# Kernel tuning notes

Hardware: AMD Instinct MI355X
Metric: run time of the kernel (lower is better)

Reference implementation:

```python
import jax, jax.numpy as jnp
import numpy as np

N = 50000
E = 800000
IN_DIM = 128
HID = 128
HEADS = 8
OUT_DIM = 64
NEG_SLOPE = 0.2


def setup_inputs() -> dict:
    key = jax.random.key(0)
    ks = jax.random.split(key, 12)
    x = jax.random.normal(ks[0], (N, IN_DIM), dtype=jnp.float32)
    edge_index = jax.random.randint(ks[1], (2, E), 0, N, dtype=jnp.int64)
    C1 = HID // HEADS  # per-head out dim of layer 1
    s1 = 1.0 / np.sqrt(IN_DIM)
    s2 = 1.0 / np.sqrt(HID)
    W1 = jax.random.uniform(ks[2], (IN_DIM, HEADS * C1), jnp.float32, -s1, s1)
    a_src1 = jax.random.uniform(ks[3], (HEADS, C1), jnp.float32, -1.0, 1.0)
    a_dst1 = jax.random.uniform(ks[4], (HEADS, C1), jnp.float32, -1.0, 1.0)
    b1 = jnp.zeros((HEADS * C1,), jnp.float32)
    W2 = jax.random.uniform(ks[5], (HID, OUT_DIM), jnp.float32, -s2, s2)
    a_src2 = jax.random.uniform(ks[6], (1, OUT_DIM), jnp.float32, -1.0, 1.0)
    a_dst2 = jax.random.uniform(ks[7], (1, OUT_DIM), jnp.float32, -1.0, 1.0)
    b2 = jnp.zeros((OUT_DIM,), jnp.float32)
    return {"x": x, "edge_index": edge_index, "W1": W1, "a_src1": a_src1,
            "a_dst1": a_dst1, "b1": b1, "W2": W2, "a_src2": a_src2,
            "a_dst2": a_dst2, "b2": b2}


def gat_conv(x, src, dst, W, a_s, a_d, b, n_heads, c_head):
    # Linear projection per head: [N, H, C]
    h = (x @ W).reshape(N, n_heads, c_head)
    # Per-node attention terms: [N, H]
    alpha_s = jnp.einsum('nhc,hc->nh', h, a_s)
    alpha_d = jnp.einsum('nhc,hc->nh', h, a_d)
    # Per-edge raw scores: [Etot, H]
    score = jax.nn.leaky_relu(alpha_s[src] + alpha_d[dst], negative_slope=NEG_SLOPE)
    # Segment softmax over edges sharing the same destination
    m = jax.ops.segment_max(score, dst, num_segments=N)
    e = jnp.exp(score - m[dst])
    denom = jax.ops.segment_sum(e, dst, num_segments=N)
    alpha = e / denom[dst]  # every node has a self-loop -> denom > 0
    # Weighted aggregation: scatter-add alpha * h_src into destinations
    out = jax.ops.segment_sum(alpha[:, :, None] * h[src], dst, num_segments=N)
    return out.reshape(N, n_heads * c_head) + b


def reference(x, edge_index, W1, a_src1, a_dst1, b1, W2, a_src2, a_dst2, b2):
    # add self loops (GATConv add_self_loops=True)
    loops = jnp.arange(N, dtype=edge_index.dtype)
    src = jnp.concatenate([edge_index[0], loops])
    dst = jnp.concatenate([edge_index[1], loops])
    C1 = HID // HEADS
    h = gat_conv(x, src, dst, W1, a_src1, a_dst1, b1, HEADS, C1)
    h = jax.nn.elu(h)  # dropout = 0 (eval)
    out = gat_conv(h, src, dst, W2, a_src2, a_dst2, b2, 1, OUT_DIM)
    return jax.nn.log_softmax(out, axis=-1)
```

## Files before the change

kernel.cpp:

```cpp
#include <hip/hip_runtime.h>
#include <math.h>

typedef unsigned int  u32;
typedef unsigned short u16;
typedef unsigned char u8;
typedef short bf16x8 __attribute__((ext_vector_type(8)));
typedef float f32x4  __attribute__((ext_vector_type(4)));
typedef float f32x2  __attribute__((ext_vector_type(2)));

#define NN    50000
#define NE    800000
#define ET    (NE + NN)
#define IND   128
#define HIDD  128
#define NH    8
#define OD    64
#define SLOPE 0.2f

#define NB    196
#define EPB   4096
#define NBB   ((NE + EPB - 1) / EPB)
#define LCAP  64
#define CAPB  5120
#define CPAD  16
#define BSTRIDE 7168

#define W1EXT 144
#define W2EXT 80
#define WPB   112
#define G1B   391

__device__ __forceinline__ u32 bf16rne(float f) {
    u32 u = __float_as_uint(f);
    return (u + 0x7fffu + ((u >> 16) & 1u)) >> 16;
}

#define LR(s) fmaxf((s), SLOPE * (s))

__global__ __launch_bounds__(256) void k_prep_bin(
    const int* __restrict__ ei, int* __restrict__ cnt, u32* __restrict__ staging,
    const float* __restrict__ W1, const float* __restrict__ W2,
    const float* __restrict__ as1w, const float* __restrict__ ad1w,
    const float* __restrict__ as2w, const float* __restrict__ ad2w,
    u16* __restrict__ Wt1, u16* __restrict__ Wt2,
    u32* __restrict__ h1f8, float* __restrict__ as1, float* __restrict__ as2)
{
    __shared__ u32 lbuf[NB * LCAP];
    __shared__ int lcnt[NB];
    __shared__ int gbase[NB];
    const int t = threadIdx.x;

    if (blockIdx.x >= NBB) {
        const int i = (blockIdx.x - NBB) * 256 + t;
        if (i < 32) h1f8[(size_t)NN * 32 + i] = 0;
        if (i < 8)  as1[(size_t)NH * NN + i] = -1e30f;
        if (i == 8) as2[NN] = -1e30f;

        if (i < W1EXT * 128) {
            const int j = i >> 7, k = i & 127;
            float v;
            if (j < 128) {
                v = W1[k * 128 + j];
            } else if (j < 136) {
                const int h = j - 128;
                v = 0.f;
                for (int c = 0; c < 16; ++c)
                    v += W1[k * 128 + h * 16 + c] * as1w[h * 16 + c];
            } else {
                const int h = j - 136;
                v = 0.f;
                for (int c = 0; c < 16; ++c)
                    v += W1[k * 128 + h * 16 + c] * ad1w[h * 16 + c];
            }
            Wt1[j * 128 + k] = (u16)bf16rne(v);
        } else if (i < W1EXT * 128 + W2EXT * 128) {
            const int i2 = i - W1EXT * 128;
            const int j = i2 >> 7, k = i2 & 127;
            float v = 0.f;
            if (j < 64) {
                v = W2[k * 64 + j];
            } else if (j == 64) {
                for (int c = 0; c < 64; ++c) v += W2[k * 64 + c] * as2w[c];
            } else if (j == 65) {
                for (int c = 0; c < 64; ++c) v += W2[k * 64 + c] * ad2w[c];
            }
            Wt2[j * 128 + k] = (u16)bf16rne(v);
        }
        return;
    }

    const int e0 = blockIdx.x * EPB;
    for (int i = t; i < NB; i += 256) lcnt[i] = 0;
    __syncthreads();

    for (int i = t; i < EPB; i += 256) {
        const int e = e0 + i;
        if (e >= NE) break;
        const int src = ei[e];
        const int dst = ei[NE + e];
        const int b = dst >> 8;
        const int p = atomicAdd(&lcnt[b], 1);
        lbuf[b * LCAP + p] = ((u32)(dst & 255) << 16) | (u32)src;
    }
    __syncthreads();

    for (int i = t; i < NB; i += 256)
        gbase[i] = atomicAdd(&cnt[i * CPAD], lcnt[i]);
    __syncthreads();

    for (int b = t; b < NB; b += 256) {
        const int n = lcnt[b];
        const int gb = gbase[b];
        u32* dstp = staging + (size_t)b * CAPB + gb;
        const u32* srcp = lbuf + b * LCAP;
        for (int j = 0; j < n; ++j) dstp[j] = srcp[j];
    }
}

__global__ __launch_bounds__(512) void k_place_gemm1(
    const int* __restrict__ cnt, const u32* __restrict__ staging,
    int* __restrict__ rowptr, int* __restrict__ rowend,
    u16* __restrict__ sorted16,
    const float* __restrict__ x, const u16* __restrict__ Wt1,
    u32* __restrict__ h1f8, float* __restrict__ as1, float* __restrict__ ad1)
{
    __shared__ u32 xb[128 * 64];
    __shared__ u32 Wb[W1EXT * 64];
    const int tid = threadIdx.x;

    if (blockIdx.x < NB) {
        int* hist = (int*)xb;
        int* cur  = hist + 256;
        int* scan = cur + 256;
        const int b = blockIdx.x;
        const int tot = cnt[b * CPAD];
        const int base = b * BSTRIDE;

        if (tid < 256) hist[tid] = ((b * 256 + tid) < NN) ? 1 : 0;
        __syncthreads();

        for (int i = tid; i < tot; i += 512)
            atomicAdd(&hist[staging[(size_t)b * CAPB + i] >> 16], 1);
        __syncthreads();

        if (tid < 256) scan[tid] = (hist[tid] + 7) & ~7;
        __syncthreads();
        for (int off = 1; off < 256; off <<= 1) {
            int v = 0;
            if (tid < 256 && tid >= off) v = scan[tid - off];
            __syncthreads();
            if (tid < 256) scan[tid] += v;
            __syncthreads();
        }
        if (tid < 256) {
            const int padded = (hist[tid] + 7) & ~7;
            const int excl = (tid == 0) ? 0 : scan[tid - 1];
            const int node = b * 256 + tid;
            if (node < NN) {
                rowptr[node] = base + excl;
                rowend[node] = base + excl + padded;
                sorted16[base + excl] = (u16)node;
                for (int j = hist[tid]; j < padded; ++j)
                    sorted16[base + excl + j] = (u16)NN;
                cur[tid] = excl + 1;
            } else {
                cur[tid] = excl;
            }
        }
        __syncthreads();
        for (int i = tid; i < tot; i += 512) {
            const u32 v = staging[(size_t)b * CAPB + i];
            const int pos = atomicAdd(&cur[v >> 16], 1);
            sorted16[base + pos] = (u16)(v & 0xffffu);
        }
        return;
    }

    const int row0 = (blockIdx.x - NB) * 128;

    {
        const uint4* Wt = (const uint4*)Wt1;
        for (int p = 0; p < 5; ++p) {
            const int id = p * 512 + tid;
            if (id < W1EXT * 16) {
                const int n = id >> 4, c = id & 15;
                *(uint4*)(Wb + n * 64 + ((c ^ (n & 15)) << 2)) = Wt[n * 16 + c];
            }
        }
    }
    for (int p = 0; p < 4; ++p) {
        const int id = p * 512 + tid;
        const int m = id >> 4, c = id & 15;
        const int row = row0 + m;
        uint4 v = make_uint4(0, 0, 0, 0);
        if (row < NN) {
            const float4 f0 = *(const float4*)(x + (size_t)row * 128 + c * 8);
            const float4 f1 = *(const float4*)(x + (size_t)row * 128 + c * 8 + 4);
            v.x = bf16rne(f0.x) | (bf16rne(f0.y) << 16);
            v.y = bf16rne(f0.z) | (bf16rne(f0.w) << 16);
            v.z = bf16rne(f1.x) | (bf16rne(f1.y) << 16);
            v.w = bf16rne(f1.z) | (bf16rne(f1.w) << 16);
        }
        *(uint4*)(xb + m * 64 + ((c ^ (m & 15)) << 2)) = v;
    }
    __syncthreads();

    const int w = tid >> 6, lane = tid & 63;
    const int nl = lane & 15, quad = lane >> 4;
    f32x4 acc[9] = {};
    for (int kk = 0; kk < 4; ++kk) {
        const int cm = kk * 4 + quad;
        const bf16x8 a = *(const bf16x8*)(xb + (16 * w + nl) * 64 + ((cm ^ nl) << 2));
#pragma unroll
        for (int tn = 0; tn < 9; ++tn) {
            const bf16x8 b = *(const bf16x8*)(Wb + (16 * tn + nl) * 64 + ((cm ^ nl) << 2));
            acc[tn] = __builtin_amdgcn_mfma_f32_16x16x32_bf16(a, b, acc[tn], 0, 0, 0);
        }
    }

    __syncthreads();
    {
        u8* h1ld = (u8*)xb;
#pragma unroll
        for (int tn = 0; tn < 8; ++tn) {
#pragma unroll
            for (int r = 0; r < 4; ++r) {
                const int row = 16 * w + quad * 4 + r;
                const u32 pk = __builtin_amdgcn_cvt_pk_fp8_f32(
                    acc[tn][r], 0.f, 0u, false);
                h1ld[row * 128 + ((tn ^ ((row >> 2) & 7)) << 4) + nl] = (u8)pk;
            }
        }
    }
#pragma unroll
    for (int r = 0; r < 4; ++r) {
        const int row = row0 + 16 * w + quad * 4 + r;
        if (row < NN) {
            const float v = acc[8][r];
            if (nl < 8) as1[row * NH + nl] = v;
            else        ad1[row * NH + (nl - 8)] = v;
        }
    }
    __syncthreads();
    for (int p = 0; p < 2; ++p) {
        const int id = p * 512 + tid;
        const int row = id >> 3, c = id & 7;
        const int grow = row0 + row;
        if (grow < NN)
            ((uint4*)h1f8)[(size_t)grow * 8 + c] =
                ((const uint4*)xb)[row * 8 + (c ^ ((row >> 2) & 7))];
    }
}

__global__ __launch_bounds__(512) void k_gemm2(
    const u32* __restrict__ act2b, const u16* __restrict__ Wt2,
    u16* __restrict__ h2s, float* __restrict__ as2, float* __restrict__ ad2)
{
    __shared__ u32 xb[128 * 64];
    __shared__ u32 Wb[W2EXT * 64];
    const int tid = threadIdx.x;
    const int row0 = blockIdx.x * 128;

    {
        const uint4* Wt = (const uint4*)Wt2;
        for (int p = 0; p < 3; ++p) {
            const int id = p * 512 + tid;
            if (id < W2EXT * 16) {
                const int n = id >> 4, c = id & 15;
                *(uint4*)(Wb + n * 64 + ((c ^ (n & 15)) << 2)) = Wt[n * 16 + c];
            }
        }
    }
    for (int p = 0; p < 4; ++p) {
        const int id = p * 512 + tid;
        const int m = id >> 4, c = id & 15;
        const int row = row0 + m;
        uint4 v = make_uint4(0, 0, 0, 0);
        if (row < NN) v = ((const uint4*)act2b)[(size_t)row * 16 + c];
        *(uint4*)(xb + m * 64 + ((c ^ (m & 15)) << 2)) = v;
    }
    __syncthreads();

    const int w = tid >> 6, lane = tid & 63;
    const int nl = lane & 15, quad = lane >> 4;
    f32x4 acc[5] = {};
    for (int kk = 0; kk < 4; ++kk) {
        const int cm = kk * 4 + quad;
        const bf16x8 a = *(const bf16x8*)(xb + (16 * w + nl) * 64 + ((cm ^ nl) << 2));
#pragma unroll
        for (int tn = 0; tn < 5; ++tn) {
            const bf16x8 b = *(const bf16x8*)(Wb + (16 * tn + nl) * 64 + ((cm ^ nl) << 2));
            acc[tn] = __builtin_amdgcn_mfma_f32_16x16x32_bf16(a, b, acc[tn], 0, 0, 0);
        }
    }

    __syncthreads();
    {
        u16* h2ld = (u16*)xb;
#pragma unroll
        for (int tn = 0; tn < 4; ++tn) {
#pragma unroll
            for (int r = 0; r < 4; ++r) {
                const int row = 16 * w + quad * 4 + r;
                h2ld[row * 64 + 16 * tn + nl] = (u16)bf16rne(acc[tn][r]);
            }
        }
    }
#pragma unroll
    for (int r = 0; r < 4; ++r) {
        const int row = row0 + 16 * w + quad * 4 + r;
        if (row < NN) {
            const float v = acc[4][r];
            if (nl == 0) as2[row] = v;
            else if (nl == 1) ad2[row] = v;
        }
    }
    __syncthreads();
    for (int p = 0; p < 2; ++p) {
        const int id = p * 512 + tid;
        const int row = id >> 3, c = id & 7;
        const int grow = row0 + row;
        if (grow < NN)
            ((uint4*)h2s)[(size_t)grow * 8 + c] = ((const uint4*)xb)[row * 8 + c];
    }
}

#define PG1(KK, S, G, WJ) do {                                                \
    const uint4 p = *(const uint4*)(sorted16 + (KK));                         \
    S[0] = p.x & 0xffffu; S[1] = p.x >> 16;                                   \
    S[2] = p.y & 0xffffu; S[3] = p.y >> 16;                                   \
    S[4] = p.z & 0xffffu; S[5] = p.z >> 16;                                   \
    S[6] = p.w & 0xffffu; S[7] = p.w >> 16;                                   \
    const u32 hlf = (head & 4) ? ((head & 2) ? p.w : p.z)                     \
                               : ((head & 2) ? p.y : p.x);                    \
    const u32 sj = (head & 1) ? (hlf >> 16) : (hlf & 0xffffu);                \
    WJ = __expf(LR(as1[sj * NH + eh] + adeh));                                \
    denacc += WJ;                                                             \
    _Pragma("unroll") for (int j = 0; j < 8; ++j)                             \
        G[j] = h1u16[S[j] * 64 + lane];                                       \
} while (0)

#define CONS1(G, WJ) do {                                                     \
    _Pragma("unroll") for (int j = 0; j < 8; ++j) {                           \
        const float wv = __uint_as_float((u32)__builtin_amdgcn_ds_bpermute(   \
            h4 + j * 32, (int)__float_as_uint(WJ)));                          \
        const f32x2 f = __builtin_amdgcn_cvt_pk_f32_fp8((u32)G[j], false);    \
        acc2 += f * wv; }                                                     \
} while (0)

__global__ __launch_bounds__(256) void k_agg1(
    const int* __restrict__ rowptr, const int* __restrict__ rowend,
    const u16* __restrict__ sorted16,
    const u16* __restrict__ h1u16, const float* __restrict__ as1,
    const float* __restrict__ ad1,
    u32* __restrict__ act2b)
{
    const int node = blockIdx.x * 4 + (threadIdx.x >> 6);
    const int lane = threadIdx.x & 63;
    const int head = lane >> 3;
    const int eh   = lane & 7;
    const float adeh = ad1[node * NH + eh];
    const int k0 = rowptr[node], kend = rowend[node];
    const int h4 = head << 2;
    f32x2 acc2 = {0.f, 0.f};
    float denacc = 0.f;
    u32 sA[8], sB[8];
    u16 gA[8], gB[8];
    float wA, wB;

    PG1(k0, sA, gA, wA);
    int k = k0 + 8;
    while (k + 16 <= kend) {
        PG1(k, sB, gB, wB);      CONS1(gA, wA);
        PG1(k + 8, sA, gA, wA);  CONS1(gB, wB);
        k += 16;
    }
    if (k < kend) {
        PG1(k, sB, gB, wB);  CONS1(gA, wA);  CONS1(gB, wB);
    } else {
        CONS1(gA, wA);
    }

    denacc += __shfl_xor(denacc, 8);
    denacc += __shfl_xor(denacc, 16);
    denacc += __shfl_xor(denacc, 32);
    const float den = __uint_as_float((u32)__builtin_amdgcn_ds_bpermute(
        h4, (int)__float_as_uint(denacc)));

    const float inv = 1.f / den;
    float v0 = acc2.x * inv, v1 = acc2.y * inv;
    v0 = v0 > 0.f ? v0 : expm1f(v0);
    v1 = v1 > 0.f ? v1 : expm1f(v1);
    act2b[node * 64 + lane] = bf16rne(v0) | (bf16rne(v1) << 16);
}

#define PG2(KK, S, G, WJ) do {                                                \
    const uint4 p = *(const uint4*)(sorted16 + (KK));                         \
    S[0] = p.x & 0xffffu; S[1] = p.x >> 16;                                   \
    S[2] = p.y & 0xffffu; S[3] = p.y >> 16;                                   \
    S[4] = p.z & 0xffffu; S[5] = p.z >> 16;                                   \
    S[6] = p.w & 0xffffu; S[7] = p.w >> 16;                                   \
    const u32 hlf2 = (lane & 4) ? ((lane & 2) ? p.w : p.z)                    \
                                : ((lane & 2) ? p.y : p.x);                   \
    const u32 sj = (lane & 1) ? (hlf2 >> 16) : (hlf2 & 0xffffu);              \
    WJ = __expf(LR(as2[sj] + adv));                                           \
    denacc += WJ;                                                             \
    _Pragma("unroll") for (int j = 0; j < 8; ++j)                             \
        G[j] = h2s[S[j] * 64 + lane];                                         \
} while (0)

#define CONS2(G, WJ) do {                                                     \
    _Pragma("unroll") for (int j = 0; j < 8; ++j) {                           \
        const float wv = __uint_as_float((u32)__builtin_amdgcn_ds_bpermute(   \
            j << 2, (int)__float_as_uint(WJ)));                               \
        acc += wv * __uint_as_float(((u32)G[j]) << 16); }                     \
} while (0)

__global__ __launch_bounds__(256) void k_agg2(
    const int* __restrict__ rowptr, const int* __restrict__ rowend,
    const u16* __restrict__ sorted16,
    const u16* __restrict__ h2s, const float* __restrict__ as2,
    const float* __restrict__ ad2,
    float* __restrict__ out)
{
    const int node = blockIdx.x * 4 + (threadIdx.x >> 6);
    const int lane = threadIdx.x & 63;
    const float adv = ad2[node];
    const int k0 = rowptr[node], kend = rowend[node];
    float acc = 0.f, denacc = 0.f;
    u32 sA[8], sB[8];
    u16 gA[8], gB[8];
    float wA, wB;

    PG2(k0, sA, gA, wA);
    int k = k0 + 8;
    while (k + 16 <= kend) {
        PG2(k, sB, gB, wB);      CONS2(gA, wA);
        PG2(k + 8, sA, gA, wA);  CONS2(gB, wB);
        k += 16;
    }
    if (k < kend) {
        PG2(k, sB, gB, wB);  CONS2(gA, wA);  CONS2(gB, wB);
    } else {
        CONS2(gA, wA);
    }

    denacc += __shfl_xor(denacc, 1);
    denacc += __shfl_xor(denacc, 2);
    denacc += __shfl_xor(denacc, 4);

    const float v = acc / denacc;
    float m = v;
    for (int kk = 1; kk < 64; kk <<= 1) m = fmaxf(m, __shfl_xor(m, kk));
    float se = __expf(v - m);
    for (int kk = 1; kk < 64; kk <<= 1) se += __shfl_xor(se, kk);
    out[node * 64 + lane] = v - m - logf(se);
}

extern "C" void kernel_launch(void* const* d_in, const int* in_sizes, int n_in,
                              void* d_out, int out_size, void* d_ws, size_t ws_size,
                              hipStream_t stream)
{
    (void)in_sizes; (void)n_in; (void)out_size; (void)ws_size;
    const float* x    = (const float*)d_in[0];
    const int*   ei   = (const int*)d_in[1];
    const float* W1   = (const float*)d_in[2];
    const float* as1w = (const float*)d_in[3];
    const float* ad1w = (const float*)d_in[4];
    const float* W2   = (const float*)d_in[6];
    const float* as2w = (const float*)d_in[7];
    const float* ad2w = (const float*)d_in[8];
    float* out = (float*)d_out;

    u32* ws = (u32*)d_ws;
    size_t o = 0;
    auto take = [&](size_t n) { size_t r = o; o += (n + 15) & ~(size_t)15; return r; };

    u32*   h1f8     = ws + take((size_t)32 * (NN + 1));
    float* as1      = (float*)(ws + take((size_t)NH * NN + 8));
    float* ad1      = (float*)(ws + take((size_t)NH * NN));
    u32*   act2b    = ws + take((size_t)64 * NN);
    float* as2      = (float*)(ws + take(NN + 1));
    float* ad2      = (float*)(ws + take(NN));
    int*   rowptr   = (int*)(ws + take(NN));
    int*   rowend   = (int*)(ws + take(NN));
    u16*   sorted16 = (u16*)(ws + take(((size_t)NB * BSTRIDE + 1) / 2));
    u32*   staging  = ws + take((size_t)NB * CAPB);
    int*   cnt      = (int*)(ws + take(NB * CPAD));
    u16*   Wt1      = (u16*)(ws + take((size_t)W1EXT * 128 / 2));
    u16*   Wt2      = (u16*)(ws + take((size_t)W2EXT * 128 / 2));
    u16*   h1u16    = (u16*)h1f8;
    u16*   h2s      = (u16*)h1f8;

    hipMemsetAsync(cnt, 0, NB * CPAD * sizeof(int), stream);

    k_prep_bin<<<NBB + WPB, 256, 0, stream>>>(
        ei, cnt, staging, W1, W2, as1w, ad1w, as2w, ad2w,
        Wt1, Wt2, h1f8, as1, as2);

    k_place_gemm1<<<NB + G1B, 512, 0, stream>>>(
        cnt, staging, rowptr, rowend, sorted16, x, Wt1, h1f8, as1, ad1);

    k_agg1<<<NN / 4, 256, 0, stream>>>(rowptr, rowend, sorted16, h1u16, as1, ad1, act2b);
    k_gemm2<<<G1B, 512, 0, stream>>>(act2b, Wt2, h2s, as2, ad2);
    k_agg2<<<NN / 4, 256, 0, stream>>>(rowptr, rowend, sorted16, h2s, as2, ad2, out);
}
```

Before: 174.7 us.

## Split wave into two edge halves with wider 32-bit gathers in aggregation

Both aggregation kernels now assign each half-wave (32 lanes) to a different edge of each 8-edge group, and each lane gathers a 32-bit word (4 fp8 or 2 bf16 values) instead of a 16-bit one. This halves the number of gather instructions per edge and widens each memory access. The two halves' partial sums are combined at the end with one cross-half shuffle, and only the lower half writes output. The cost is the extra reduction, some lanes idle at the final store, and more complex weight broadcasts through bpermute.

```diff
diff --git a/kernel.cpp b/kernel.cpp
--- a/kernel.cpp
+++ b/kernel.cpp
@@ -325,58 +325,66 @@
     }
 }
 
-#define PG1(KK, S, G, WJ) do {                                                \
-    const uint4 p = *(const uint4*)(sorted16 + (KK));                         \
-    S[0] = p.x & 0xffffu; S[1] = p.x >> 16;                                   \
-    S[2] = p.y & 0xffffu; S[3] = p.y >> 16;                                   \
-    S[4] = p.z & 0xffffu; S[5] = p.z >> 16;                                   \
-    S[6] = p.w & 0xffffu; S[7] = p.w >> 16;                                   \
-    const u32 hlf = (head & 4) ? ((head & 2) ? p.w : p.z)                     \
-                               : ((head & 2) ? p.y : p.x);                    \
-    const u32 sj = (head & 1) ? (hlf >> 16) : (hlf & 0xffffu);                \
+#define PG1(KK, P, G, WJ) do {                                                \
+    P = *(const uint4*)(sorted16 + (KK));                                     \
+    const u32 hlf = (ej & 4) ? ((ej & 2) ? P.w : P.z)                         \
+                             : ((ej & 2) ? P.y : P.x);                        \
+    const u32 sj = (ej & 1) ? (hlf >> 16) : (hlf & 0xffffu);                  \
     WJ = __expf(LR(as1[sj * NH + eh] + adeh));                                \
     denacc += WJ;                                                             \
-    _Pragma("unroll") for (int j = 0; j < 8; ++j)                             \
-        G[j] = h1u16[S[j] * 64 + lane];                                       \
+    const u32 s0 = (P.x >> hsh) & 0xffffu;                                    \
+    const u32 s1 = (P.y >> hsh) & 0xffffu;                                    \
+    const u32 s2 = (P.z >> hsh) & 0xffffu;                                    \
+    const u32 s3 = (P.w >> hsh) & 0xffffu;                                    \
+    G[0] = h1u32[(size_t)s0 * 32 + q];                                        \
+    G[1] = h1u32[(size_t)s1 * 32 + q];                                        \
+    G[2] = h1u32[(size_t)s2 * 32 + q];                                        \
+    G[3] = h1u32[(size_t)s3 * 32 + q];                                        \
 } while (0)
 
 #define CONS1(G, WJ) do {                                                     \
-    _Pragma("unroll") for (int j = 0; j < 8; ++j) {                           \
+    _Pragma("unroll") for (int i = 0; i < 4; ++i) {                           \
         const float wv = __uint_as_float((u32)__builtin_amdgcn_ds_bpermute(   \
-            h4 + j * 32, (int)__float_as_uint(WJ)));                          \
-        const f32x2 f = __builtin_amdgcn_cvt_pk_f32_fp8((u32)G[j], false);    \
-        acc2 += f * wv; }                                                     \
+            bpb + (i << 6), (int)__float_as_uint(WJ)));                       \
+        const f32x2 flo = __builtin_amdgcn_cvt_pk_f32_fp8(G[i], false);       \
+        const f32x2 fhi = __builtin_amdgcn_cvt_pk_f32_fp8(G[i], true);        \
+        accA += flo * wv;                                                     \
+        accB += fhi * wv; }                                                   \
 } while (0)
 
 __global__ __launch_bounds__(256) void k_agg1(
     const int* __restrict__ rowptr, const int* __restrict__ rowend,
     const u16* __restrict__ sorted16,
-    const u16* __restrict__ h1u16, const float* __restrict__ as1,
+    const u32* __restrict__ h1u32, const float* __restrict__ as1,
     const float* __restrict__ ad1,
     u32* __restrict__ act2b)
 {
     const int node = blockIdx.x * 4 + (threadIdx.x >> 6);
     const int lane = threadIdx.x & 63;
-    const int head = lane >> 3;
-    const int eh   = lane & 7;
+    const int ej = lane >> 3;
+    const int eh = lane & 7;
     const float adeh = ad1[node * NH + eh];
+    const int half = lane >> 5;
+    const int hsh  = half << 4;
+    const int q    = lane & 31;
+    const int bpb  = (half << 5) | ((q >> 2) << 2);
+    const int gh4  = (q >> 2) << 2;
     const int k0 = rowptr[node], kend = rowend[node];
-    const int h4 = head << 2;
-    f32x2 acc2 = {0.f, 0.f};
+    f32x2 accA = {0.f, 0.f}, accB = {0.f, 0.f};
     float denacc = 0.f;
-    u32 sA[8], sB[8];
-    u16 gA[8], gB[8];
+    uint4 pA, pB;
+    u32 gA[4], gB[4];
     float wA, wB;
 
-    PG1(k0, sA, gA, wA);
+    PG1(k0, pA, gA, wA);
     int k = k0 + 8;
     while (k + 16 <= kend) {
-        PG1(k, sB, gB, wB);      CONS1(gA, wA);
-        PG1(k + 8, sA, gA, wA);  CONS1(gB, wB);
+        PG1(k, pB, gB, wB);      CONS1(gA, wA);
+        PG1(k + 8, pA, gA, wA);  CONS1(gB, wB);
         k += 16;
     }
     if (k < kend) {
-        PG1(k, sB, gB, wB);  CONS1(gA, wA);  CONS1(gB, wB);
+        PG1(k, pB, gB, wB);  CONS1(gA, wA);  CONS1(gB, wB);
     } else {
         CONS1(gA, wA);
     }
@@ -385,62 +393,83 @@
     denacc += __shfl_xor(denacc, 16);
     denacc += __shfl_xor(denacc, 32);
     const float den = __uint_as_float((u32)__builtin_amdgcn_ds_bpermute(
-        h4, (int)__float_as_uint(denacc)));
+        gh4, (int)__float_as_uint(denacc)));
+
+    accA.x += __shfl_xor(accA.x, 32);
+    accA.y += __shfl_xor(accA.y, 32);
+    accB.x += __shfl_xor(accB.x, 32);
+    accB.y += __shfl_xor(accB.y, 32);
 
     const float inv = 1.f / den;
-    float v0 = acc2.x * inv, v1 = acc2.y * inv;
+    float v0 = accA.x * inv, v1 = accA.y * inv;
+    float v2 = accB.x * inv, v3 = accB.y * inv;
     v0 = v0 > 0.f ? v0 : expm1f(v0);
     v1 = v1 > 0.f ? v1 : expm1f(v1);
-    act2b[node * 64 + lane] = bf16rne(v0) | (bf16rne(v1) << 16);
-}
-
-#define PG2(KK, S, G, WJ) do {                                                \
-    const uint4 p = *(const uint4*)(sorted16 + (KK));                         \
-    S[0] = p.x & 0xffffu; S[1] = p.x >> 16;                                   \
-    S[2] = p.y & 0xffffu; S[3] = p.y >> 16;                                   \
-    S[4] = p.z & 0xffffu; S[5] = p.z >> 16;                                   \
-    S[6] = p.w & 0xffffu; S[7] = p.w >> 16;                                   \
-    const u32 hlf2 = (lane & 4) ? ((lane & 2) ? p.w : p.z)                    \
-                                : ((lane & 2) ? p.y : p.x);                   \
+    v2 = v2 > 0.f ? v2 : expm1f(v2);
+    v3 = v3 > 0.f ? v3 : expm1f(v3);
+    if (lane < 32) {
+        uint2 o;
+        o.x = bf16rne(v0) | (bf16rne(v1) << 16);
+        o.y = bf16rne(v2) | (bf16rne(v3) << 16);
+        *(uint2*)(act2b + (size_t)node * 64 + q * 2) = o;
+    }
+}
+
+#define PG2(KK, P, G, WJ) do {                                                \
+    P = *(const uint4*)(sorted16 + (KK));                                     \
+    const u32 hlf2 = (lane & 4) ? ((lane & 2) ? P.w : P.z)                    \
+                                : ((lane & 2) ? P.y : P.x);                   \
     const u32 sj = (lane & 1) ? (hlf2 >> 16) : (hlf2 & 0xffffu);              \
     WJ = __expf(LR(as2[sj] + adv));                                           \
     denacc += WJ;                                                             \
-    _Pragma("unroll") for (int j = 0; j < 8; ++j)                             \
-        G[j] = h2s[S[j] * 64 + lane];                                         \
+    const u32 s0 = (P.x >> hsh) & 0xffffu;                                    \
+    const u32 s1 = (P.y >> hsh) & 0xffffu;                                    \
+    const u32 s2 = (P.z >> hsh) & 0xffffu;                                    \
+    const u32 s3 = (P.w >> hsh) & 0xffffu;                                    \
+    G[0] = h2u32[(size_t)s0 * 32 + chp];                                      \
+    G[1] = h2u32[(size_t)s1 * 32 + chp];                                      \
+    G[2] = h2u32[(size_t)s2 * 32 + chp];                                      \
+    G[3] = h2u32[(size_t)s3 * 32 + chp];                                      \
 } while (0)
 
 #define CONS2(G, WJ) do {                                                     \
-    _Pragma("unroll") for (int j = 0; j < 8; ++j) {                           \
+    _Pragma("unroll") for (int i = 0; i < 4; ++i) {                           \
         const float wv = __uint_as_float((u32)__builtin_amdgcn_ds_bpermute(   \
-            j << 2, (int)__float_as_uint(WJ)));                               \
-        acc += wv * __uint_as_float(((u32)G[j]) << 16); }                     \
+            bph + (i << 3), (int)__float_as_uint(WJ)));                       \
+        acc2.x += wv * __uint_as_float(G[i] << 16);                           \
+        acc2.y += wv * __uint_as_float(G[i] & 0xffff0000u); }                 \
 } while (0)
 
 __global__ __launch_bounds__(256) void k_agg2(
     const int* __restrict__ rowptr, const int* __restrict__ rowend,
     const u16* __restrict__ sorted16,
-    const u16* __restrict__ h2s, const float* __restrict__ as2,
+    const u32* __restrict__ h2u32, const float* __restrict__ as2,
     const float* __restrict__ ad2,
     float* __restrict__ out)
 {
     const int node = blockIdx.x * 4 + (threadIdx.x >> 6);
     const int lane = threadIdx.x & 63;
     const float adv = ad2[node];
+    const int half = lane >> 5;
+    const int hsh  = half << 4;
+    const int chp  = lane & 31;
+    const int bph  = half << 2;
     const int k0 = rowptr[node], kend = rowend[node];
-    float acc = 0.f, denacc = 0.f;
-    u32 sA[8], sB[8];
-    u16 gA[8], gB[8];
+    f32x2 acc2 = {0.f, 0.f};
+    float denacc = 0.f;
+    uint4 pA, pB;
+    u32 gA[4], gB[4];
     float wA, wB;
 
-    PG2(k0, sA, gA, wA);
+    PG2(k0, pA, gA, wA);
     int k = k0 + 8;
     while (k + 16 <= kend) {
-        PG2(k, sB, gB, wB);      CONS2(gA, wA);
-        PG2(k + 8, sA, gA, wA);  CONS2(gB, wB);
+        PG2(k, pB, gB, wB);      CONS2(gA, wA);
+        PG2(k + 8, pA, gA, wA);  CONS2(gB, wB);
         k += 16;
     }
     if (k < kend) {
-        PG2(k, sB, gB, wB);  CONS2(gA, wA);  CONS2(gB, wB);
+        PG2(k, pB, gB, wB);  CONS2(gA, wA);  CONS2(gB, wB);
     } else {
         CONS2(gA, wA);
     }
@@ -449,12 +478,28 @@
     denacc += __shfl_xor(denacc, 2);
     denacc += __shfl_xor(denacc, 4);
 
-    const float v = acc / denacc;
-    float m = v;
-    for (int kk = 1; kk < 64; kk <<= 1) m = fmaxf(m, __shfl_xor(m, kk));
-    float se = __expf(v - m);
-    for (int kk = 1; kk < 64; kk <<= 1) se += __shfl_xor(se, kk);
-    out[node * 64 + lane] = v - m - logf(se);
+    acc2.x += __shfl_xor(acc2.x, 32);
+    acc2.y += __shfl_xor(acc2.y, 32);
+
+    const float inv = 1.f / denacc;
+    const float v0 = acc2.x * inv, v1 = acc2.y * inv;
+    float m = fmaxf(v0, v1);
+    m = fmaxf(m, __shfl_xor(m, 1));
+    m = fmaxf(m, __shfl_xor(m, 2));
+    m = fmaxf(m, __shfl_xor(m, 4));
+    m = fmaxf(m, __shfl_xor(m, 8));
+    m = fmaxf(m, __shfl_xor(m, 16));
+    float se = __expf(v0 - m) + __expf(v1 - m);
+    se += __shfl_xor(se, 1);
+    se += __shfl_xor(se, 2);
+    se += __shfl_xor(se, 4);
+    se += __shfl_xor(se, 8);
+    se += __shfl_xor(se, 16);
+    const float lse = m + logf(se);
+    if (lane < 32) {
+        float2 o = make_float2(v0 - lse, v1 - lse);
+        *(float2*)(out + (size_t)node * 64 + chp * 2) = o;
+    }
 }
 
 extern "C" void kernel_launch(void* const* d_in, const int* in_sizes, int n_in,
@@ -489,8 +534,8 @@
     int*   cnt      = (int*)(ws + take(NB * CPAD));
     u16*   Wt1      = (u16*)(ws + take((size_t)W1EXT * 128 / 2));
     u16*   Wt2      = (u16*)(ws + take((size_t)W2EXT * 128 / 2));
-    u16*   h1u16    = (u16*)h1f8;
     u16*   h2s      = (u16*)h1f8;
+    u32*   h2u32    = h1f8;
 
     hipMemsetAsync(cnt, 0, NB * CPAD * sizeof(int), stream);
 
@@ -501,7 +546,7 @@
     k_place_gemm1<<<NB + G1B, 512, 0, stream>>>(
         cnt, staging, rowptr, rowend, sorted16, x, Wt1, h1f8, as1, ad1);
 
-    k_agg1<<<NN / 4, 256, 0, stream>>>(rowptr, rowend, sorted16, h1u16, as1, ad1, act2b);
+    k_agg1<<<NN / 4, 256, 0, stream>>>(rowptr, rowend, sorted16, h1f8, as1, ad1, act2b);
     k_gemm2<<<G1B, 512, 0, stream>>>(act2b, Wt2, h2s, as2, ad2);
-    k_agg2<<<NN / 4, 256, 0, stream>>>(rowptr, rowend, sorted16, h2s, as2, ad2, out);
-}
+    k_agg2<<<NN / 4, 256, 0, stream>>>(rowptr, rowend, sorted16, h2u32, as2, ad2, out);
+}
```

Result: no change. 173.1 us (-0.9%).
